# Performance work log

Hardware: AMD Instinct MI355X
Metric: run time of the kernel (lower is better)

The kernel has to match this reference:

```python
import jax, jax.numpy as jnp
import numpy as np

B, T, E, H, NH, L, R, K, N, P, HOR = 32, 16, 768, 1024, 16, 6, 8, 16, 100000, 9, 8
HD = H // NH


def _ln(x, g, b):
    m = jnp.mean(x, -1, keepdims=True)
    v = jnp.mean((x - m) ** 2, -1, keepdims=True)
    return (x - m) * jax.lax.rsqrt(v + 1e-5) * g + b


def _lora(x, W, A, Bm, b):
    # base linear + low-rank update: x W^T + (x A^T) B^T + b
    return x @ W.T + (x @ A.T) @ Bm.T + b


def setup_inputs() -> dict:
    key = jax.random.key(0)
    ks = iter(jax.random.split(key, 64))
    def rn(shape, s):
        return jax.random.normal(next(ks), shape, dtype=jnp.float32) * s
    d = {}
    d['history_img_emb'] = rn((B, T, E), 1.0)
    d['current_emb'] = rn((B, E), 1.0)
    d['goal_emb'] = rn((B, E), 1.0)
    d['subgoal_emb'] = rn((B, E), 1.0)
    d['beacon_emb'] = rn((B, E), 1.0)
    d['history_proprio'] = rn((B, T, P), 1.0)
    d['proprio'] = rn((B, P), 1.0)
    d['bank'] = rn((N, E), 1.0)
    d['hp_W'] = rn((H, E + P), 0.02); d['hp_b'] = jnp.zeros((H,), jnp.float32)
    d['ip_W'] = rn((H, E), 0.02); d['ip_b'] = jnp.zeros((H,), jnp.float32)
    d['pp_W'] = rn((H, P), 0.02); d['pp_b'] = jnp.zeros((H,), jnp.float32)
    d['plan_token'] = rn((1, 1, H), 0.02)
    d['ln1_g'] = jnp.ones((L, H), jnp.float32); d['ln1_b'] = jnp.zeros((L, H), jnp.float32)
    d['ln2_g'] = jnp.ones((L, H), jnp.float32); d['ln2_b'] = jnp.zeros((L, H), jnp.float32)
    for nm, o, i in (('q', H, H), ('k', H, H), ('v', H, H), ('o', H, H), ('f1', 4 * H, H), ('f2', H, 4 * H)):
        d[nm + 'W'] = rn((L, o, i), 0.02)
        d[nm + 'A'] = rn((L, R, i), 0.02)
        d[nm + 'B'] = rn((L, o, R), 0.02)
        d[nm + 'b'] = jnp.zeros((L, o), jnp.float32)
    d['fln_g'] = jnp.ones((H,), jnp.float32); d['fln_b'] = jnp.zeros((H,), jnp.float32)
    d['ah_W1'] = rn((H, H), 0.02); d['ah_b1'] = jnp.zeros((H,), jnp.float32)
    d['ah_W2'] = rn((3, H), 0.02); d['ah_b2'] = jnp.zeros((3,), jnp.float32)
    d['rh_W1'] = rn((H, H + 3), 0.02); d['rh_b1'] = jnp.zeros((H,), jnp.float32)
    d['rh_W2'] = rn((HOR * 3, H), 0.02); d['rh_b2'] = jnp.zeros((HOR * 3,), jnp.float32)
    d['sh_W'] = rn((1, H), 0.02); d['sh_b'] = jnp.zeros((1,), jnp.float32)
    return d


def reference(history_img_emb, current_emb, goal_emb, subgoal_emb, beacon_emb,
              history_proprio, proprio, bank,
              hp_W, hp_b, ip_W, ip_b, pp_W, pp_b, plan_token,
              ln1_g, ln1_b, ln2_g, ln2_b,
              qW, qA, qB, qb, kW, kA, kB, kb, vW, vA, vB, vb, oW, oA, oB, ob,
              f1W, f1A, f1B, f1b, f2W, f2A, f2B, f2b,
              fln_g, fln_b, ah_W1, ah_b1, ah_W2, ah_b2,
              rh_W1, rh_b1, rh_W2, rh_b2, sh_W, sh_b):
    # batched semantic-bank top-k retrieval (replaces the per-sample python loop)
    sims = current_emb @ bank.T                      # [B, N]
    scores, idx = jax.lax.top_k(sims, K)             # [B, K]
    sem = bank[idx] * scores[..., None]              # [B, K, E] gather + scale

    # multi-modal token fusion
    hist = jnp.concatenate([history_img_emb, history_proprio], -1) @ hp_W.T + hp_b  # [B, T, H]
    img = lambda e: e @ ip_W.T + ip_b
    goal_t = img(goal_emb)[:, None]
    sub_t = img(subgoal_emb)[:, None]
    bea_t = img(beacon_emb)[:, None]
    sem_t = img(sem)                                 # [B, K, H]
    prop_t = (proprio @ pp_W.T + pp_b)[:, None]
    plan_t = jnp.broadcast_to(plan_token, (B, 1, H))
    x = jnp.concatenate([plan_t, hist, goal_t, sub_t, bea_t, sem_t, prop_t], 1)  # [B, S=37, H]

    scale = 1.0 / np.sqrt(HD).astype(np.float32)
    for l in range(L):
        h = _ln(x, ln1_g[l], ln1_b[l])
        q = _lora(h, qW[l], qA[l], qB[l], qb[l]).reshape(B, -1, NH, HD)
        k = _lora(h, kW[l], kA[l], kB[l], kb[l]).reshape(B, -1, NH, HD)
        v = _lora(h, vW[l], vA[l], vB[l], vb[l]).reshape(B, -1, NH, HD)
        attn = jax.nn.softmax(jnp.einsum('bshd,bthd->bhst', q, k) * scale, axis=-1)
        out = jnp.einsum('bhst,bthd->bshd', attn, v).reshape(B, -1, H)
        x = x + _lora(out, oW[l], oA[l], oB[l], ob[l])
        h2 = _ln(x, ln2_g[l], ln2_b[l])
        x = x + _lora(jax.nn.gelu(_lora(h2, f1W[l], f1A[l], f1B[l], f1b[l]), approximate=False),
                      f2W[l], f2A[l], f2B[l], f2b[l])

    x = _ln(x, fln_g, fln_b)
    ps = x[:, 0]                                     # plan token state [B, H]
    anchor = jax.nn.gelu(ps @ ah_W1.T + ah_b1, approximate=False) @ ah_W2.T + ah_b2  # [B, 3]
    ref_in = jnp.concatenate([ps, anchor], -1)
    waypoints = (jax.nn.gelu(ref_in @ rh_W1.T + rh_b1, approximate=False) @ rh_W2.T + rh_b2).reshape(B, HOR, 3)
    stop_logit = (ps @ sh_W.T + sh_b)[:, 0]          # [B]
    return anchor, waypoints, stop_logit
```

## Files before the change

### kernel.cpp

```cpp
#include <hip/hip_runtime.h>
#include <float.h>
#include <math.h>

#define NB 100000
#define SEQ 37
#define NTOK 1184
#define TKCH 16

typedef __attribute__((ext_vector_type(8))) short short8;
typedef __attribute__((ext_vector_type(4))) float floatx4;

__device__ __forceinline__ short f2bf(float f) {
  union { float f; unsigned u; } x; x.f = f;
  unsigned r = x.u + 0x7fff + ((x.u >> 16) & 1);
  return (short)(r >> 16);
}

__device__ __forceinline__ float gelu_f(float v) {
  return 0.5f * v * (1.f + erff(v * 0.70710678118654752f));
}

__global__ __launch_bounds__(256) void wconv_all(const float* __restrict__ qW,
                                                 const float* __restrict__ kW,
                                                 const float* __restrict__ vW,
                                                 const float* __restrict__ oW,
                                                 const float* __restrict__ f1W,
                                                 const float* __restrict__ f2W,
                                                 short* __restrict__ wb) {
  const int l = blockIdx.x / 1536;
  const int t = blockIdx.x - l * 1536;
  const float* src; int Kd; size_t doff; int np, kc;
  if (t < 512) {
    const int w = t >> 7, ti = t & 127;
    const float* base = (w == 0) ? qW : (w == 1) ? kW : (w == 2) ? vW : oW;
    src = base + (size_t)l * 1024 * 1024;
    Kd = 1024; np = ti >> 4; kc = ti & 15;
    doff = (size_t)w * 1048576 + ((size_t)np * 16 + kc) * 8192;
  } else if (t < 1024) {
    const int ti = t - 512;
    src = f1W + (size_t)l * 4096 * 1024;
    Kd = 1024; np = ti >> 4; kc = ti & 15;
    doff = (size_t)4 * 1048576 + ((size_t)np * 16 + kc) * 8192;
  } else {
    const int ti = t - 1024;
    src = f2W + (size_t)l * 1024 * 4096;
    Kd = 4096; np = ti >> 6; kc = ti & 63;
    doff = (size_t)8 * 1048576 + ((size_t)np * 64 + kc) * 8192;
  }
  short* dst = wb + (size_t)l * 12 * 1048576 + doff;
  const float* sp = src + (size_t)(np * 128) * Kd + kc * 64;
  const int tid = threadIdx.x;
#pragma unroll
  for (int q = 0; q < 4; ++q) {
    const int d = q * 256 + tid;
    const int row = d >> 3, slot = d & 7;
    const int ss = slot ^ (row & 7);
    const float* s = sp + (size_t)row * Kd + ss * 8;
    const float4 u0 = *(const float4*)s;
    const float4 u1 = *(const float4*)(s + 4);
    short8 v;
    v[0] = f2bf(u0.x); v[1] = f2bf(u0.y); v[2] = f2bf(u0.z); v[3] = f2bf(u0.w);
    v[4] = f2bf(u1.x); v[5] = f2bf(u1.y); v[6] = f2bf(u1.z); v[7] = f2bf(u1.w);
    *(short8*)(dst + (size_t)d * 8) = v;
  }
}

__global__ __launch_bounds__(256) void wconv_embed(const float* __restrict__ hpW,
                                                   const float* __restrict__ ipW,
                                                   short* __restrict__ wbe) {
  const int t = blockIdx.x;
  const float* src; int Kd, np, kc; size_t doff;
  if (t < 104) { src = hpW; Kd = 777; np = t / 13; kc = t - np * 13; doff = (size_t)t * 8192; }
  else { const int ti = t - 104; src = ipW; Kd = 768; np = ti / 12; kc = ti - np * 12;
         doff = (size_t)t * 8192; }
  short* dst = wbe + doff;
  const int tid = threadIdx.x;
#pragma unroll
  for (int q = 0; q < 4; ++q) {
    const int d = q * 256 + tid;
    const int row = d >> 3, slot = d & 7;
    const int ss = slot ^ (row & 7);
    const int gk0 = kc * 64 + ss * 8;
    const float* s = src + (size_t)(np * 128 + row) * Kd;
    short8 v;
#pragma unroll
    for (int e = 0; e < 8; ++e) v[e] = (gk0 + e < Kd) ? f2bf(s[gk0 + e]) : (short)0;
    *(short8*)(dst + (size_t)d * 8) = v;
  }
}

__global__ __launch_bounds__(256) void gemm_bt(const float* __restrict__ A, int lda,
                                               const short* __restrict__ WT, size_t wzstride,
                                               const float* __restrict__ b0,
                                               const float* __restrict__ b1,
                                               const float* __restrict__ b2,
                                               const float* __restrict__ LT,
                                               const float* __restrict__ B0,
                                               const float* __restrict__ B1,
                                               const float* __restrict__ B2,
                                               float* __restrict__ C, size_t czstride,
                                               int ldc, int M, int K,
                                               int acc_flag, int gelu_flag,
                                               int ksn, float* __restrict__ part) {
  __shared__ short Al[2][64 * 64];
  __shared__ short Wl[2][128 * 64];
  const int z = blockIdx.z;
  const int kidx = (ksn > 1) ? z : 0;
  const float* bias = (ksn > 1 || z == 0) ? b0 : (z == 1) ? b1 : b2;
  const float* Bz = (ksn > 1 || z == 0) ? B0 : (z == 1) ? B1 : B2;
  if (ksn == 1) C += (size_t)z * czstride;
  const int nkc_tot = K >> 6;
  const int nkc = nkc_tot / ksn;
  const short* wt = WT + (size_t)((ksn > 1) ? 0 : z) * wzstride +
                    ((size_t)blockIdx.y * nkc_tot + (size_t)kidx * nkc) * 8192;
  const int tid = threadIdx.x;
  const int wid = tid >> 6, lane = tid & 63;
  const int wr = wid >> 1, wc = wid & 1;
  const int bm = blockIdx.x * 64, bn = blockIdx.y * 128;
  const int arow = tid >> 2;
  const int s0 = (tid & 3) * 2;

  floatx4 acc[2][4];
#pragma unroll
  for (int i = 0; i < 2; ++i)
#pragma unroll
    for (int j = 0; j < 4; ++j)
#pragma unroll
      for (int r = 0; r < 4; ++r) acc[i][j][r] = 0.f;

  const int ga = bm + arow;
  const bool aok = ga < M;
  const float* ap = A + (size_t)ga * lda + (size_t)kidx * nkc * 64;
  const int aswz = arow & 7;

  float4 ar[4];
  short8 wreg[4];

#define LOAD_A(kc_)                                                        \
  {                                                                        \
    _Pragma("unroll") for (int j = 0; j < 2; ++j) {                        \
      const int slot = s0 + j;                                             \
      if (aok) {                                                           \
        ar[j * 2] = *(const float4*)(ap + (kc_)*64 + slot * 8);            \
        ar[j * 2 + 1] = *(const float4*)(ap + (kc_)*64 + slot * 8 + 4);    \
      } else {                                                             \
        ar[j * 2] = make_float4(0.f, 0.f, 0.f, 0.f);                      \
        ar[j * 2 + 1] = make_float4(0.f, 0.f, 0.f, 0.f);                  \
      }                                                                    \
    }                                                                      \
  }
#define LOAD_W(kc_)                                                        \
  {                                                                        \
    _Pragma("unroll") for (int it = 0; it < 4; ++it)                       \
        wreg[it] = *(const short8*)(wt + (size_t)(kc_)*8192 + (it * 256 + tid) * 8); \
  }
#define WRITE_A(buf_)                                                      \
  {                                                                        \
    _Pragma("unroll") for (int j = 0; j < 2; ++j) {                        \
      const int slot = s0 + j;                                             \
      short8 s;                                                            \
      s[0] = f2bf(ar[j * 2].x); s[1] = f2bf(ar[j * 2].y);                  \
      s[2] = f2bf(ar[j * 2].z); s[3] = f2bf(ar[j * 2].w);                  \
      s[4] = f2bf(ar[j * 2 + 1].x); s[5] = f2bf(ar[j * 2 + 1].y);          \
      s[6] = f2bf(ar[j * 2 + 1].z); s[7] = f2bf(ar[j * 2 + 1].w);          \
      *(short8*)&Al[buf_][arow * 64 + ((slot ^ aswz) << 3)] = s;           \
    }                                                                      \
  }
#define WRITE_W(buf_)                                                      \
  {                                                                        \
    _Pragma("unroll") for (int it = 0; it < 4; ++it)                       \
        *(short8*)&Wl[buf_][(it * 256 + tid) * 8] = wreg[it];              \
  }

  LOAD_W(0) LOAD_A(0)
  WRITE_A(0) WRITE_W(0)
  __syncthreads();

  for (int t = 0; t < nkc; ++t) {
    const int cur = t & 1, nxt = cur ^ 1;
    const bool more = (t + 1 < nkc);
    if (more) { LOAD_W(t + 1) LOAD_A(t + 1) }
#pragma unroll
    for (int ks = 0; ks < 2; ++ks) {
      short8 af[2], wf[4];
#pragma unroll
      for (int i = 0; i < 2; ++i) {
        const int row = wr * 32 + i * 16 + (lane & 15);
        const int sa = (ks * 4 + (lane >> 4)) ^ (row & 7);
        af[i] = *(const short8*)&Al[cur][row * 64 + sa * 8];
      }
#pragma unroll
      for (int j = 0; j < 4; ++j) {
        const int col = wc * 64 + j * 16 + (lane & 15);
        const int sw2 = (ks * 4 + (lane >> 4)) ^ (col & 7);
        wf[j] = *(const short8*)&Wl[cur][col * 64 + sw2 * 8];
      }
#pragma unroll
      for (int i = 0; i < 2; ++i)
#pragma unroll
        for (int j = 0; j < 4; ++j)
          acc[i][j] = __builtin_amdgcn_mfma_f32_16x16x32_bf16(af[i], wf[j], acc[i][j], 0, 0, 0);
    }
    if (more) { WRITE_A(nxt) WRITE_W(nxt) }
    __syncthreads();
  }
#undef LOAD_A
#undef LOAD_W
#undef WRITE_A
#undef WRITE_W

  if (ksn > 1) {
#pragma unroll
    for (int i = 0; i < 2; ++i) {
      const int gm0 = bm + wr * 32 + i * 16 + (lane >> 4) * 4;
#pragma unroll
      for (int r = 0; r < 4; ++r) {
        const int gm = gm0 + r;
        if (gm >= M) continue;
#pragma unroll
        for (int j = 0; j < 4; ++j) {
          const int gn = bn + wc * 64 + j * 16 + (lane & 15);
          part[((size_t)kidx * M + gm) * ldc + gn] = acc[i][j][r];
        }
      }
    }
    return;
  }

  float br[4][8];
  if (LT) {
#pragma unroll
    for (int j = 0; j < 4; ++j) {
      const int gn = bn + wc * 64 + j * 16 + (lane & 15);
      const float4 u0 = *(const float4*)(Bz + (size_t)gn * 8);
      const float4 u1 = *(const float4*)(Bz + (size_t)gn * 8 + 4);
      br[j][0] = u0.x; br[j][1] = u0.y; br[j][2] = u0.z; br[j][3] = u0.w;
      br[j][4] = u1.x; br[j][5] = u1.y; br[j][6] = u1.z; br[j][7] = u1.w;
    }
  }
#pragma unroll
  for (int i = 0; i < 2; ++i) {
    const int gm0 = bm + wr * 32 + i * 16 + (lane >> 4) * 4;
#pragma unroll
    for (int r = 0; r < 4; ++r) {
      const int gm = gm0 + r;
      if (gm >= M) continue;
      float lt[8];
      if (LT) {
        const float4 t0 = *(const float4*)(LT + ((size_t)z * NTOK + gm) * 8);
        const float4 t1 = *(const float4*)(LT + ((size_t)z * NTOK + gm) * 8 + 4);
        lt[0] = t0.x; lt[1] = t0.y; lt[2] = t0.z; lt[3] = t0.w;
        lt[4] = t1.x; lt[5] = t1.y; lt[6] = t1.z; lt[7] = t1.w;
      }
#pragma unroll
      for (int j = 0; j < 4; ++j) {
        const int gn = bn + wc * 64 + j * 16 + (lane & 15);
        float o = acc[i][j][r] + bias[gn];
        if (LT)
          o += lt[0] * br[j][0] + lt[1] * br[j][1] + lt[2] * br[j][2] + lt[3] * br[j][3] +
               lt[4] * br[j][4] + lt[5] * br[j][5] + lt[6] * br[j][6] + lt[7] * br[j][7];
        const size_t off = (size_t)gm * ldc + gn;
        if (acc_flag) o += C[off];
        if (gelu_flag) o = gelu_f(o);
        C[off] = o;
      }
    }
  }
}

__global__ __launch_bounds__(256) void reduce_ks(const float* __restrict__ part,
                                                 const float* __restrict__ bias,
                                                 const float* __restrict__ LT,
                                                 const float* __restrict__ Bm,
                                                 float* __restrict__ X, int KS) {
  const int idx = blockIdx.x * 256 + threadIdx.x;
  if (idx >= NTOK * 1024) return;
  const int gm = idx >> 10, gn = idx & 1023;
  float s = 0.f;
  for (int h = 0; h < KS; ++h) s += part[(size_t)h * NTOK * 1024 + idx];
  const float* t = LT + (size_t)gm * 8;
  const float* bp = Bm + (size_t)gn * 8;
  s += t[0] * bp[0] + t[1] * bp[1] + t[2] * bp[2] + t[3] * bp[3] +
       t[4] * bp[4] + t[5] * bp[5] + t[6] * bp[6] + t[7] * bp[7];
  X[idx] += s + bias[gn];
}

__global__ __launch_bounds__(256) void redln(const float* __restrict__ part, int KS,
                                             const float* __restrict__ bias,
                                             const float* __restrict__ Bm,
                                             float* __restrict__ X,
                                             float* __restrict__ out,
                                             const float* __restrict__ g,
                                             const float* __restrict__ bt,
                                             const float* __restrict__ A0,
                                             const float* __restrict__ A1,
                                             const float* __restrict__ A2,
                                             int nz, float* __restrict__ lt) {
  __shared__ float red[4];
  __shared__ float red2[4][8];
  const int row = blockIdx.x, tid = threadIdx.x;
  const int wave = tid >> 6, lane = tid & 63;
  float ltv[8];
  {
    const float4 t0 = *(const float4*)(lt + (size_t)row * 8);
    const float4 t1 = *(const float4*)(lt + (size_t)row * 8 + 4);
    ltv[0] = t0.x; ltv[1] = t0.y; ltv[2] = t0.z; ltv[3] = t0.w;
    ltv[4] = t1.x; ltv[5] = t1.y; ltv[6] = t1.z; ltv[7] = t1.w;
  }
  float v[4];
#pragma unroll
  for (int i = 0; i < 4; ++i) {
    const int c = tid + 256 * i;
    float s = 0.f;
    for (int h = 0; h < KS; ++h)
      s += part[((size_t)h * NTOK + row) * 1024 + c];
    const float* bp = Bm + (size_t)c * 8;
    s += ltv[0] * bp[0] + ltv[1] * bp[1] + ltv[2] * bp[2] + ltv[3] * bp[3] +
         ltv[4] * bp[4] + ltv[5] * bp[5] + ltv[6] * bp[6] + ltv[7] * bp[7];
    float xnew = X[(size_t)row * 1024 + c] + s + bias[c];
    X[(size_t)row * 1024 + c] = xnew;
    v[i] = xnew;
  }
  float sum = v[0] + v[1] + v[2] + v[3];
#pragma unroll
  for (int s = 32; s; s >>= 1) sum += __shfl_down(sum, s);
  if ((tid & 63) == 0) red[tid >> 6] = sum;
  __syncthreads();
  float mean = (red[0] + red[1] + red[2] + red[3]) * (1.f / 1024.f);
  __syncthreads();
  float sq = 0.f;
#pragma unroll
  for (int i = 0; i < 4; ++i) { float d = v[i] - mean; sq += d * d; }
#pragma unroll
  for (int s = 32; s; s >>= 1) sq += __shfl_down(sq, s);
  if ((tid & 63) == 0) red[tid >> 6] = sq;
  __syncthreads();
  float var = (red[0] + red[1] + red[2] + red[3]) * (1.f / 1024.f);
  float inv = rsqrtf(var + 1e-5f);
  float* orow = out + (size_t)row * 1024;
  float nv[4];
#pragma unroll
  for (int i = 0; i < 4; ++i) {
    const int c = tid + 256 * i;
    nv[i] = (v[i] - mean) * inv * g[c] + bt[c];
    orow[c] = nv[i];
  }
  __syncthreads();
  for (int z = 0; z < nz; ++z) {
    const float* Am = (z == 0) ? A0 : (z == 1) ? A1 : A2;
    float p[8];
#pragma unroll
    for (int r = 0; r < 8; ++r) {
      float s = 0.f;
#pragma unroll
      for (int i = 0; i < 4; ++i) s += nv[i] * Am[r * 1024 + tid + 256 * i];
      p[r] = s;
    }
#pragma unroll
    for (int sh = 1; sh < 64; sh <<= 1) {
#pragma unroll
      for (int r = 0; r < 8; ++r) p[r] += __shfl_xor(p[r], sh);
    }
    if (lane == 0) {
#pragma unroll
      for (int r = 0; r < 8; ++r) red2[wave][r] = p[r];
    }
    __syncthreads();
    if (tid < 8)
      lt[((size_t)z * NTOK + row) * 8 + tid] =
          red2[0][tid] + red2[1][tid] + red2[2][tid] + red2[3][tid];
    __syncthreads();
  }
}

__global__ __launch_bounds__(256) void gemm_sm2(const float* __restrict__ A, int lda,
                                                const float* __restrict__ W, int ldw,
                                                const float* __restrict__ bias,
                                                float* __restrict__ C, int ldc,
                                                float* __restrict__ part,
                                                int N, int K, int gelu_flag) {
  __shared__ float buf[8192];
  const int tid = threadIdx.x;
  const int col = tid >> 3, ksub = tid & 7;
  const int gcol = blockIdx.x * 32 + col;
  const int KS = gridDim.y, ky = blockIdx.y;
  const int kchunk = (((K + KS - 1) / KS) + 127) & ~127;
  const int kstart = ky * kchunk;
  const int kend = (kstart + kchunk < K) ? (kstart + kchunk) : K;
  const float* wp = W + (size_t)(gcol < N ? gcol : 0) * ldw;

  float acc[32];
#pragma unroll
  for (int m = 0; m < 32; ++m) acc[m] = 0.f;

  for (int kc = kstart; kc < kend; kc += 128) {
    __syncthreads();
#pragma unroll
    for (int q = 0; q < 4; ++q) {
      const int idx4 = q * 256 + tid;
      const int m = idx4 >> 5, j = (idx4 & 31) * 4;
      const int gk = kc + j;
      float4 v;
      if (gk + 3 < K) {
        v = *(const float4*)(A + (size_t)m * lda + gk);
      } else {
        v.x = (gk < K) ? A[(size_t)m * lda + gk] : 0.f;
        v.y = (gk + 1 < K) ? A[(size_t)m * lda + gk + 1] : 0.f;
        v.z = (gk + 2 < K) ? A[(size_t)m * lda + gk + 2] : 0.f;
        v.w = (gk + 3 < K) ? A[(size_t)m * lda + gk + 3] : 0.f;
      }
      *(float4*)&buf[m * 128 + j] = v;
    }
    __syncthreads();
#pragma unroll
    for (int kk = 0; kk < 4; ++kk) {
      const int j = kk * 32 + ksub * 4;
      const int gk = kc + j;
      float4 w4 = make_float4(0.f, 0.f, 0.f, 0.f);
      if (gcol < N && gk < K) {
        if (gk + 3 < K) {
          w4 = *(const float4*)(wp + gk);
        } else {
          w4.x = wp[gk];
          if (gk + 1 < K) w4.y = wp[gk + 1];
          if (gk + 2 < K) w4.z = wp[gk + 2];
        }
      }
#pragma unroll
      for (int m = 0; m < 32; ++m) {
        const float4 a4 = *(const float4*)&buf[m * 128 + j];
        acc[m] += a4.x * w4.x + a4.y * w4.y + a4.z * w4.z + a4.w * w4.w;
      }
    }
  }
  __syncthreads();
#pragma unroll
  for (int m = 0; m < 32; ++m) buf[m * 256 + ksub * 32 + col] = acc[m];
  __syncthreads();
#pragma unroll
  for (int g = 0; g < 4; ++g) {
    const int idx = g * 256 + tid;
    const int m = idx >> 5, c = idx & 31;
    float s = 0.f;
#pragma unroll
    for (int h = 0; h < 8; ++h) s += buf[m * 256 + h * 32 + c];
    const int gc = blockIdx.x * 32 + c;
    if (gc < N) {
      if (KS == 1) {
        float o = s + bias[gc];
        if (gelu_flag) o = gelu_f(o);
        C[(size_t)m * ldc + gc] = o;
      } else {
        part[((size_t)ky * 32 + m) * N + gc] = s;
      }
    }
  }
}

__global__ __launch_bounds__(256) void reduce_sm(const float* __restrict__ part,
                                                 const float* __restrict__ bias,
                                                 float* __restrict__ C, int ldc,
                                                 int N, int KS, int gelu_flag) {
  const int idx = blockIdx.x * 256 + threadIdx.x;
  if (idx >= 32 * N) return;
  const int m = idx / N, c = idx - m * N;
  float s = 0.f;
  for (int h = 0; h < KS; ++h) s += part[((size_t)h * 32 + m) * N + c];
  float o = s + bias[c];
  if (gelu_flag) o = gelu_f(o);
  C[(size_t)m * ldc + c] = o;
}

__global__ __launch_bounds__(256) void sims_kernel(const float* __restrict__ cur,
                                                   const float* __restrict__ bank,
                                                   float* __restrict__ sims) {
  __shared__ float Bs[32][132];
  __shared__ float Cs[32][36];
  const int tid = threadIdx.x;
  const int tx = tid & 7;
  const int ty = tid >> 3;
  const int n0 = blockIdx.x * 128;
  const int srow = tid >> 1;
  const int spart = tid & 1;
  const int cb = tid >> 3;
  const int ck = (tid & 7) * 4;

  float acc[4][4] = {{0.f,0.f,0.f,0.f},{0.f,0.f,0.f,0.f},
                     {0.f,0.f,0.f,0.f},{0.f,0.f,0.f,0.f}};

  const bool rok = (n0 + srow) < NB;
  const float* bp = bank + (size_t)(n0 + srow) * 768 + spart * 16;
  const float* cp = cur + (size_t)cb * 768 + ck;

  for (int kc = 0; kc < 768; kc += 32) {
    __syncthreads();
#pragma unroll
    for (int jj = 0; jj < 4; ++jj) {
      float4 v = rok ? *(const float4*)(bp + kc + jj * 4)
                     : make_float4(0.f, 0.f, 0.f, 0.f);
      const int kk = spart * 16 + jj * 4;
      Bs[kk + 0][srow] = v.x; Bs[kk + 1][srow] = v.y;
      Bs[kk + 2][srow] = v.z; Bs[kk + 3][srow] = v.w;
    }
    {
      float4 v = *(const float4*)(cp + kc);
      Cs[ck + 0][cb] = v.x; Cs[ck + 1][cb] = v.y;
      Cs[ck + 2][cb] = v.z; Cs[ck + 3][cb] = v.w;
    }
    __syncthreads();
#pragma unroll
    for (int kk = 0; kk < 32; ++kk) {
      float4 av = *(const float4*)&Bs[kk][ty * 4];
      float4 bv = *(const float4*)&Cs[kk][tx * 4];
      float a4[4] = {av.x, av.y, av.z, av.w};
      float b4[4] = {bv.x, bv.y, bv.z, bv.w};
#pragma unroll
      for (int i = 0; i < 4; ++i)
#pragma unroll
        for (int j = 0; j < 4; ++j) acc[i][j] += a4[i] * b4[j];
    }
  }
  const int n = n0 + ty * 4;
#pragma unroll
  for (int j = 0; j < 4; ++j) {
    const int b = tx * 4 + j;
    float4 o = make_float4(acc[0][j], acc[1][j], acc[2][j], acc[3][j]);
    if (n + 3 < NB) {
      *(float4*)(sims + (size_t)b * NB + n) = o;
    } else {
      float oo[4] = {o.x, o.y, o.z, o.w};
      for (int i = 0; i < 4; ++i)
        if (n + i < NB) sims[(size_t)b * NB + n + i] = oo[i];
    }
  }
}

__global__ __launch_bounds__(256) void topk_stage1(const float* __restrict__ sims,
                                                   float* __restrict__ cv,
                                                   int* __restrict__ ci) {
  __shared__ float ss[4096];
  __shared__ int si[4096];
  __shared__ float wv[4];
  __shared__ int wi[4];
  const int chunk = blockIdx.x, b = blockIdx.y, tid = threadIdx.x;
  const int start = chunk * (NB / TKCH), end = start + (NB / TKCH);
  float ls[16]; int li[16];
#pragma unroll
  for (int i = 0; i < 16; ++i) { ls[i] = -FLT_MAX; li[i] = 0x7fffffff; }
  const float* row = sims + (size_t)b * NB;
  float lmin = -FLT_MAX;
  for (int n = start + tid; n < end; n += 256) {
    float v = row[n];
    if (v > lmin) {
      int p = 15;
      while (p > 0 && ls[p - 1] < v) { ls[p] = ls[p - 1]; li[p] = li[p - 1]; --p; }
      ls[p] = v; li[p] = n;
      lmin = ls[15];
    }
  }
#pragma unroll
  for (int i = 0; i < 16; ++i) { ss[i * 256 + tid] = ls[i]; si[i * 256 + tid] = li[i]; }
  __syncthreads();
  for (int round = 0; round < 16; ++round) {
    float bv = -FLT_MAX; int bi = 0x7fffffff;
#pragma unroll
    for (int i = 0; i < 16; ++i) {
      float v = ss[i * 256 + tid]; int ix = si[i * 256 + tid];
      if (v > bv || (v == bv && ix < bi)) { bv = v; bi = ix; }
    }
#pragma unroll
    for (int s = 32; s; s >>= 1) {
      float ov = __shfl_down(bv, s); int oi = __shfl_down(bi, s);
      if (ov > bv || (ov == bv && oi < bi)) { bv = ov; bi = oi; }
    }
    if ((tid & 63) == 0) { wv[tid >> 6] = bv; wi[tid >> 6] = bi; }
    __syncthreads();
    if (tid == 0) {
      bv = wv[0]; bi = wi[0];
      for (int w = 1; w < 4; ++w)
        if (wv[w] > bv || (wv[w] == bv && wi[w] < bi)) { bv = wv[w]; bi = wi[w]; }
      cv[(b * TKCH + chunk) * 16 + round] = bv;
      ci[(b * TKCH + chunk) * 16 + round] = bi;
      wi[0] = bi;
    }
    __syncthreads();
    bi = wi[0];
#pragma unroll
    for (int i = 0; i < 16; ++i)
      if (si[i * 256 + tid] == bi) ss[i * 256 + tid] = -FLT_MAX;
    __syncthreads();
  }
}

__global__ __launch_bounds__(256) void topk_stage2(const float* __restrict__ cv,
                                                   const int* __restrict__ ci,
                                                   float* __restrict__ tks,
                                                   int* __restrict__ tki) {
  __shared__ float wv[4];
  __shared__ int wi[4];
  __shared__ int bw;
  const int b = blockIdx.x, tid = threadIdx.x;
  float val = cv[b * 256 + tid];
  int idx = ci[b * 256 + tid];
  for (int round = 0; round < 16; ++round) {
    float bv = val; int bi = idx;
#pragma unroll
    for (int s = 1; s < 64; s <<= 1) {
      float ov = __shfl_xor(bv, s); int oi = __shfl_xor(bi, s);
      if (ov > bv || (ov == bv && oi < bi)) { bv = ov; bi = oi; }
    }
    if ((tid & 63) == 0) { wv[tid >> 6] = bv; wi[tid >> 6] = bi; }
    __syncthreads();
    if (tid == 0) {
      bv = wv[0]; bi = wi[0];
      for (int w = 1; w < 4; ++w)
        if (wv[w] > bv || (wv[w] == bv && wi[w] < bi)) { bv = wv[w]; bi = wi[w]; }
      tks[b * 16 + round] = bv; tki[b * 16 + round] = bi;
      bw = bi;
    }
    __syncthreads();
    if (idx == bw) val = -FLT_MAX;
  }
}

__global__ void sem_kernel(const float* __restrict__ bank, const float* __restrict__ tks,
                           const int* __restrict__ tki, float* __restrict__ sem) {
  int slot = blockIdx.x;
  float s = tks[slot]; int idx = tki[slot];
  for (int i = threadIdx.x; i < 768; i += 256)
    sem[(size_t)slot * 768 + i] = bank[(size_t)idx * 768 + i] * s;
}

__global__ void build_hist_in(const float* __restrict__ img, const float* __restrict__ pr,
                              float* __restrict__ out) {
  int r = blockIdx.x;
  for (int i = threadIdx.x; i < 832; i += 256)
    out[(size_t)r * 832 + i] = (i < 768) ? img[(size_t)r * 768 + i]
                             : (i < 777) ? pr[r * 9 + (i - 768)] : 0.f;
}

__global__ void build_img_in(const float* __restrict__ goal, const float* __restrict__ sub,
                             const float* __restrict__ bea, float* __restrict__ out) {
  int r = blockIdx.x;
  const float* src = (r < 32) ? goal + (size_t)r * 768
                   : (r < 64) ? sub + (size_t)(r - 32) * 768
                              : bea + (size_t)(r - 64) * 768;
  for (int i = threadIdx.x; i < 768; i += 256) out[(size_t)r * 768 + i] = src[i];
}

__global__ void assemble_x(const float* __restrict__ th, const float* __restrict__ ti,
                           const float* __restrict__ tp, const float* __restrict__ plan,
                           float* __restrict__ x) {
  int r = blockIdx.x;
  int b = r / SEQ, tok = r - b * SEQ;
  const float* src;
  if (tok == 0) src = plan;
  else if (tok <= 16) src = th + (size_t)(b * 16 + tok - 1) * 1024;
  else if (tok <= 19) src = ti + (size_t)((tok - 17) * 32 + b) * 1024;
  else if (tok <= 35) src = ti + (size_t)(96 + b * 16 + (tok - 20)) * 1024;
  else src = tp + (size_t)b * 1024;
  for (int i = threadIdx.x; i < 1024; i += 256) x[(size_t)r * 1024 + i] = src[i];
}

__global__ void build_ref(const float* __restrict__ ps, const float* __restrict__ anc,
                          float* __restrict__ ref) {
  int b = blockIdx.x;
  for (int i = threadIdx.x; i < 1027; i += 256)
    ref[(size_t)b * 1027 + i] = (i < 1024) ? ps[(size_t)b * 1024 + i] : anc[b * 3 + (i - 1024)];
}

__device__ __forceinline__ float block_sum256(float v, float* red) {
#pragma unroll
  for (int s = 32; s; s >>= 1) v += __shfl_down(v, s);
  if ((threadIdx.x & 63) == 0) red[threadIdx.x >> 6] = v;
  __syncthreads();
  float tot = red[0] + red[1] + red[2] + red[3];
  __syncthreads();
  return tot;
}

__global__ __launch_bounds__(256) void ln_kernel(const float* __restrict__ in, int in_stride,
                                                 float* __restrict__ out,
                                                 const float* __restrict__ g,
                                                 const float* __restrict__ bt,
                                                 const float* __restrict__ A0,
                                                 const float* __restrict__ A1,
                                                 const float* __restrict__ A2,
                                                 int nz, float* __restrict__ lt) {
  __shared__ float red[4];
  __shared__ float red2[4][8];
  const float* xr = in + (size_t)blockIdx.x * in_stride;
  const int tid = threadIdx.x;
  const int wave = tid >> 6, lane = tid & 63;
  float v[4];
#pragma unroll
  for (int i = 0; i < 4; ++i) v[i] = xr[tid + 256 * i];
  float mean = block_sum256(v[0] + v[1] + v[2] + v[3], red) * (1.f / 1024.f);
  float sq = 0.f;
#pragma unroll
  for (int i = 0; i < 4; ++i) { float d = v[i] - mean; sq += d * d; }
  float var = block_sum256(sq, red) * (1.f / 1024.f);
  float inv = rsqrtf(var + 1e-5f);
  float* orow = out + (size_t)blockIdx.x * 1024;
  float nv[4];
#pragma unroll
  for (int i = 0; i < 4; ++i) {
    int c = tid + 256 * i;
    nv[i] = (v[i] - mean) * inv * g[c] + bt[c];
    orow[c] = nv[i];
  }
  for (int z = 0; z < nz; ++z) {
    const float* Am = (z == 0) ? A0 : (z == 1) ? A1 : A2;
    float p[8];
#pragma unroll
    for (int r = 0; r < 8; ++r) {
      float s = 0.f;
#pragma unroll
      for (int i = 0; i < 4; ++i) s += nv[i] * Am[r * 1024 + tid + 256 * i];
      p[r] = s;
    }
#pragma unroll
    for (int sh = 1; sh < 64; sh <<= 1) {
#pragma unroll
      for (int r = 0; r < 8; ++r) p[r] += __shfl_xor(p[r], sh);
    }
    if (lane == 0) {
#pragma unroll
      for (int r = 0; r < 8; ++r) red2[wave][r] = p[r];
    }
    __syncthreads();
    if (tid < 8)
      lt[((size_t)z * NTOK + blockIdx.x) * 8 + tid] =
          red2[0][tid] + red2[1][tid] + red2[2][tid] + red2[3][tid];
    __syncthreads();
  }
}

__global__ __launch_bounds__(256) void lora_down(const float* __restrict__ h,
                                                 const float* __restrict__ A0,
                                                 const float* __restrict__ A1,
                                                 const float* __restrict__ A2,
                                                 float* __restrict__ lt, int K) {
  __shared__ float red[4][8];
  const int m = blockIdx.x, z = blockIdx.y;
  const int tid = threadIdx.x, wave = tid >> 6, lane = tid & 63;
  const float* A = (z == 0) ? A0 : (z == 1) ? A1 : A2;
  float p[8] = {0.f, 0.f, 0.f, 0.f, 0.f, 0.f, 0.f, 0.f};
  for (int kk = tid; kk < K; kk += 256) {
    float hv = h[(size_t)m * K + kk];
#pragma unroll
    for (int r = 0; r < 8; ++r) p[r] += hv * A[r * K + kk];
  }
#pragma unroll
  for (int s = 1; s < 64; s <<= 1) {
#pragma unroll
    for (int r = 0; r < 8; ++r) p[r] += __shfl_xor(p[r], s);
  }
  if (lane == 0) {
#pragma unroll
    for (int r = 0; r < 8; ++r) red[wave][r] = p[r];
  }
  __syncthreads();
  if (tid < 8)
    lt[((size_t)z * NTOK + m) * 8 + tid] =
        red[0][tid] + red[1][tid] + red[2][tid] + red[3][tid];
}

__global__ __launch_bounds__(256) void attn_kernel(const float* __restrict__ q,
                                                   const float* __restrict__ k,
                                                   const float* __restrict__ v,
                                                   float* __restrict__ ao) {
  __shared__ float qs[SEQ * 64], ks[SEQ * 64], vs[SEQ * 64], sc[SEQ * 40];
  const int head = blockIdx.x, b = blockIdx.y, tid = threadIdx.x;
  const size_t base = ((size_t)b * SEQ) * 1024 + head * 64;
  for (int i = tid; i < SEQ * 64; i += 256) {
    int s = i >> 6, d = i & 63;
    size_t off = base + (size_t)s * 1024 + d;
    qs[i] = q[off]; ks[i] = k[off]; vs[i] = v[off];
  }
  __syncthreads();
  for (int p = tid; p < SEQ * SEQ; p += 256) {
    int s = p / SEQ, t = p - s * SEQ;
    float acc = 0.f;
#pragma unroll 16
    for (int d = 0; d < 64; ++d) acc += qs[s * 64 + d] * ks[t * 64 + d];
    sc[s * 40 + t] = acc * 0.125f;
  }
  __syncthreads();
  if (tid < SEQ) {
    float m = -FLT_MAX;
    for (int t = 0; t < SEQ; ++t) m = fmaxf(m, sc[tid * 40 + t]);
    float sum = 0.f;
    for (int t = 0; t < SEQ; ++t) { float e = expf(sc[tid * 40 + t] - m); sc[tid * 40 + t] = e; sum += e; }
    float inv = 1.f / sum;
    for (int t = 0; t < SEQ; ++t) sc[tid * 40 + t] *= inv;
  }
  __syncthreads();
  for (int i = tid; i < SEQ * 64; i += 256) {
    int s = i >> 6, d = i & 63;
    float acc = 0.f;
    for (int t = 0; t < SEQ; ++t) acc += sc[s * 40 + t] * vs[t * 64 + d];
    ao[base + (size_t)s * 1024 + d] = acc;
  }
}

extern "C" void kernel_launch(void* const* d_in, const int* in_sizes, int n_in,
                              void* d_out, int out_size, void* d_ws, size_t ws_size,
                              hipStream_t stream) {
  const float* hist_img = (const float*)d_in[0];
  const float* cur      = (const float*)d_in[1];
  const float* goal     = (const float*)d_in[2];
  const float* sub      = (const float*)d_in[3];
  const float* bea      = (const float*)d_in[4];
  const float* hist_pr  = (const float*)d_in[5];
  const float* prop     = (const float*)d_in[6];
  const float* bank     = (const float*)d_in[7];
  const float* hpW = (const float*)d_in[8];  const float* hpb = (const float*)d_in[9];
  const float* ipW = (const float*)d_in[10]; const float* ipb = (const float*)d_in[11];
  const float* ppW = (const float*)d_in[12]; const float* ppb = (const float*)d_in[13];
  const float* plan = (const float*)d_in[14];
  const float* ln1g = (const float*)d_in[15]; const float* ln1b = (const float*)d_in[16];
  const float* ln2g = (const float*)d_in[17]; const float* ln2b = (const float*)d_in[18];
  const float* qW = (const float*)d_in[19]; const float* qA = (const float*)d_in[20];
  const float* qB = (const float*)d_in[21]; const float* qb = (const float*)d_in[22];
  const float* kW = (const float*)d_in[23]; const float* kA = (const float*)d_in[24];
  const float* kB = (const float*)d_in[25]; const float* kb = (const float*)d_in[26];
  const float* vW = (const float*)d_in[27]; const float* vA = (const float*)d_in[28];
  const float* vB = (const float*)d_in[29]; const float* vb = (const float*)d_in[30];
  const float* oW = (const float*)d_in[31]; const float* oA = (const float*)d_in[32];
  const float* oB = (const float*)d_in[33]; const float* ob = (const float*)d_in[34];
  const float* f1W = (const float*)d_in[35]; const float* f1A = (const float*)d_in[36];
  const float* f1B = (const float*)d_in[37]; const float* f1b = (const float*)d_in[38];
  const float* f2W = (const float*)d_in[39]; const float* f2A = (const float*)d_in[40];
  const float* f2B = (const float*)d_in[41]; const float* f2b = (const float*)d_in[42];
  const float* flng = (const float*)d_in[43]; const float* flnb = (const float*)d_in[44];
  const float* ahW1 = (const float*)d_in[45]; const float* ahb1 = (const float*)d_in[46];
  const float* ahW2 = (const float*)d_in[47]; const float* ahb2 = (const float*)d_in[48];
  const float* rhW1 = (const float*)d_in[49]; const float* rhb1 = (const float*)d_in[50];
  const float* rhW2 = (const float*)d_in[51]; const float* rhb2 = (const float*)d_in[52];
  const float* shW = (const float*)d_in[53]; const float* shb = (const float*)d_in[54];
  float* out = (float*)d_out;

  float* ws  = (float*)d_ws;
  float* F1O = ws;
  float* SIMS = ws;
  float* X   = F1O + (size_t)NTOK * 4096;
  float* Hb  = X  + (size_t)NTOK * 1024;
  float* Qb  = Hb + (size_t)NTOK * 1024;
  float* Kb  = Qb + (size_t)NTOK * 1024;
  float* Vb  = Kb + (size_t)NTOK * 1024;
  float* AOb = Vb + (size_t)NTOK * 1024;
  float* LT  = AOb + (size_t)NTOK * 1024;
  float* SEM = LT + (size_t)3 * NTOK * 8;
  float* HIN = SEM + (size_t)512 * 768;
  float* TKS = HIN + (size_t)512 * 832;
  int*   TKI = (int*)(TKS + 512);
  float* PS  = TKS + 1024;
  float* HH  = PS + 32 * 1024;
  float* REF = HH + 32 * 1024;
  float* CV  = REF + 32 * 1027;
  int*   CI  = (int*)(CV + 32 * 256);
  float* PART = (float*)(CI + 32 * 256);
  float* PF2 = PART + 8 * 32 * 1024;
  short* WB  = (short*)(PF2 + (size_t)4 * NTOK * 1024);
  short* WBE = WB + (size_t)6 * 12 * 1048576;

  const size_t czs = (size_t)NTOK * 1024;
  const size_t WM = 1048576;
  const size_t WL = 12 * WM;

  auto gemms = [&](const float* A, int lda, const float* W, int ldw, const float* bias,
                   float* C, int ldc, int N, int K, int geluf, int KS) {
    gemm_sm2<<<dim3((N + 31) / 32, KS), 256, 0, stream>>>(A, lda, W, ldw, bias,
                                                          C, ldc, PART, N, K, geluf);
    if (KS > 1)
      reduce_sm<<<(32 * N + 255) / 256, 256, 0, stream>>>(PART, bias, C, ldc, N, KS, geluf);
  };

  wconv_all<<<6 * 1536, 256, 0, stream>>>(qW, kW, vW, oW, f1W, f2W, WB);
  wconv_embed<<<200, 256, 0, stream>>>(hpW, ipW, WBE);

  sims_kernel<<<(NB + 127) / 128, 256, 0, stream>>>(cur, bank, SIMS);
  topk_stage1<<<dim3(TKCH, 32), 256, 0, stream>>>(SIMS, CV, CI);
  topk_stage2<<<32, 256, 0, stream>>>(CV, CI, TKS, TKI);
  sem_kernel<<<512, 256, 0, stream>>>(bank, TKS, TKI, AOb + (size_t)96 * 768);

  build_hist_in<<<512, 256, 0, stream>>>(hist_img, hist_pr, HIN);
  build_img_in<<<96, 256, 0, stream>>>(goal, sub, bea, AOb);
  gemm_bt<<<dim3(8, 8, 1), 256, 0, stream>>>(
      HIN, 832, WBE, 0, hpb, hpb, hpb,
      nullptr, nullptr, nullptr, nullptr, Qb, 0, 1024, 512, 832, 0, 0, 1, nullptr);
  gemm_bt<<<dim3(10, 8, 1), 256, 0, stream>>>(
      AOb, 768, WBE + (size_t)104 * 8192, 0, ipb, ipb, ipb,
      nullptr, nullptr, nullptr, nullptr, Kb, 0, 1024, 608, 768, 0, 0, 1, nullptr);
  gemms(prop, 9, ppW, 9, ppb, Vb, 1024, 1024, 9, 0, 1);
  assemble_x<<<NTOK, 256, 0, stream>>>(Qb, Kb, Vb, plan, X);

  const int mblk = (NTOK + 63) / 64;
  ln_kernel<<<NTOK, 256, 0, stream>>>(X, 1024, Hb, ln1g, ln1b, qA, kA, vA, 3, LT);
  for (int l = 0; l < 6; ++l) {
    const size_t aO = (size_t)l * 8 * 1024, bO = (size_t)l * 1024 * 8,
                 biO = (size_t)l * 1024;
    const size_t a4O = (size_t)l * 8 * 4096, b4O = (size_t)l * 4096 * 8,
                 bi4O = (size_t)l * 4096;
    const short* WBl = WB + (size_t)l * WL;
    gemm_bt<<<dim3(mblk, 8, 3), 256, 0, stream>>>(
        Hb, 1024, WBl, WM, qb + biO, kb + biO, vb + biO,
        LT, qB + bO, kB + bO, vB + bO, Qb, czs, 1024, NTOK, 1024, 0, 0, 1, nullptr);
    attn_kernel<<<dim3(16, 32), 256, 0, stream>>>(Qb, Kb, Vb, AOb);
    lora_down<<<dim3(NTOK, 1), 256, 0, stream>>>(AOb, oA + aO, oA + aO, oA + aO, LT, 1024);
    gemm_bt<<<dim3(mblk, 8, 2), 256, 0, stream>>>(
        AOb, 1024, WBl + 3 * WM, 0, ob + biO, ob + biO, ob + biO,
        nullptr, nullptr, nullptr, nullptr, nullptr, 0, 1024, NTOK, 1024, 0, 0, 2, PF2);
    redln<<<NTOK, 256, 0, stream>>>(PF2, 2, ob + biO, oB + bO, X, Hb,
                                    ln2g + biO, ln2b + biO,
                                    f1A + aO, f1A + aO, f1A + aO, 1, LT);
    gemm_bt<<<dim3(mblk, 32, 1), 256, 0, stream>>>(
        Hb, 1024, WBl + 4 * WM, 0, f1b + bi4O, f1b + bi4O, f1b + bi4O,
        LT, f1B + b4O, f1B + b4O, f1B + b4O, F1O, 0, 4096, NTOK, 1024, 0, 1, 1, nullptr);
    lora_down<<<dim3(NTOK, 1), 256, 0, stream>>>(F1O, f2A + a4O, f2A + a4O, f2A + a4O, LT, 4096);
    gemm_bt<<<dim3(mblk, 8, 4), 256, 0, stream>>>(
        F1O, 4096, WBl + 8 * WM, 0, f2b + biO, f2b + biO, f2b + biO,
        nullptr, nullptr, nullptr, nullptr, nullptr, 0, 1024, NTOK, 4096, 0, 0, 4, PF2);
    if (l < 5) {
      redln<<<NTOK, 256, 0, stream>>>(PF2, 4, f2b + biO, f2B + bO, X, Hb,
                                      ln1g + biO + 1024, ln1b + biO + 1024,
                                      qA + aO + 8192, kA + aO + 8192, vA + aO + 8192,
                                      3, LT);
    } else {
      reduce_ks<<<(NTOK * 1024 + 255) / 256, 256, 0, stream>>>(PF2, f2b + biO, LT,
                                                               f2B + bO, X, 4);
    }
  }

  ln_kernel<<<32, 256, 0, stream>>>(X, SEQ * 1024, PS, flng, flnb,
                                    nullptr, nullptr, nullptr, 0, nullptr);
  gemms(PS, 1024, ahW1, 1024, ahb1, HH, 1024, 1024, 1024, 1, 8);
  gemms(HH, 1024, ahW2, 1024, ahb2, out, 3, 3, 1024, 0, 8);
  build_ref<<<32, 256, 0, stream>>>(PS, out, REF);
  gemms(REF, 1027, rhW1, 1027, rhb1, HH, 1024, 1024, 1027, 1, 8);
  gemms(HH, 1024, rhW2, 1024, rhb2, out + 96, 24, 24, 1024, 0, 8);
  gemms(PS, 1024, shW, 1024, shb, out + 864, 1, 1, 1024, 0, 8);
}
```

Before: 1.688 ms.

## Scatter embedding GEMM outputs directly into sequence layout; warp-parallel attention softmax

Result: no change. 1.694 ms (+0.4%).

```diff
diff --git a/kernel.cpp b/kernel.cpp
--- a/kernel.cpp
+++ b/kernel.cpp
@@ -101,7 +101,8 @@
                                                float* __restrict__ C, size_t czstride,
                                                int ldc, int M, int K,
                                                int acc_flag, int gelu_flag,
-                                               int ksn, float* __restrict__ part) {
+                                               int ksn, float* __restrict__ part,
+                                               int rowmap) {
   __shared__ short Al[2][64 * 64];
   __shared__ short Wl[2][128 * 64];
   const int z = blockIdx.z;
@@ -252,6 +253,13 @@
         lt[0] = t0.x; lt[1] = t0.y; lt[2] = t0.z; lt[3] = t0.w;
         lt[4] = t1.x; lt[5] = t1.y; lt[6] = t1.z; lt[7] = t1.w;
       }
+      int xr = gm;
+      if (rowmap == 1) {
+        xr = (gm >> 4) * SEQ + 1 + (gm & 15);
+      } else if (rowmap == 2) {
+        if (gm < 96) xr = (gm & 31) * SEQ + 17 + (gm >> 5);
+        else { const int jj = gm - 96; xr = (jj >> 4) * SEQ + 20 + (jj & 15); }
+      }
 #pragma unroll
       for (int j = 0; j < 4; ++j) {
         const int gn = bn + wc * 64 + j * 16 + (lane & 15);
@@ -259,7 +267,7 @@
         if (LT)
           o += lt[0] * br[j][0] + lt[1] * br[j][1] + lt[2] * br[j][2] + lt[3] * br[j][3] +
                lt[4] * br[j][4] + lt[5] * br[j][5] + lt[6] * br[j][6] + lt[7] * br[j][7];
-        const size_t off = (size_t)gm * ldc + gn;
+        const size_t off = (size_t)xr * ldc + gn;
         if (acc_flag) o += C[off];
         if (gelu_flag) o = gelu_f(o);
         C[off] = o;
@@ -648,18 +656,10 @@
   for (int i = threadIdx.x; i < 768; i += 256) out[(size_t)r * 768 + i] = src[i];
 }
 
-__global__ void assemble_x(const float* __restrict__ th, const float* __restrict__ ti,
-                           const float* __restrict__ tp, const float* __restrict__ plan,
-                           float* __restrict__ x) {
-  int r = blockIdx.x;
-  int b = r / SEQ, tok = r - b * SEQ;
-  const float* src;
-  if (tok == 0) src = plan;
-  else if (tok <= 16) src = th + (size_t)(b * 16 + tok - 1) * 1024;
-  else if (tok <= 19) src = ti + (size_t)((tok - 17) * 32 + b) * 1024;
-  else if (tok <= 35) src = ti + (size_t)(96 + b * 16 + (tok - 20)) * 1024;
-  else src = tp + (size_t)b * 1024;
-  for (int i = threadIdx.x; i < 1024; i += 256) x[(size_t)r * 1024 + i] = src[i];
+__global__ void plan_fill(const float* __restrict__ plan, float* __restrict__ x) {
+  int b = blockIdx.x;
+  for (int i = threadIdx.x; i < 1024; i += 256)
+    x[((size_t)b * SEQ) * 1024 + i] = plan[i];
 }
 
 __global__ void build_ref(const float* __restrict__ ps, const float* __restrict__ anc,
@@ -772,6 +772,7 @@
                                                    float* __restrict__ ao) {
   __shared__ float qs[SEQ * 64], ks[SEQ * 64], vs[SEQ * 64], sc[SEQ * 40];
   const int head = blockIdx.x, b = blockIdx.y, tid = threadIdx.x;
+  const int wave = tid >> 6, lane = tid & 63;
   const size_t base = ((size_t)b * SEQ) * 1024 + head * 64;
   for (int i = tid; i < SEQ * 64; i += 256) {
     int s = i >> 6, d = i & 63;
@@ -787,13 +788,16 @@
     sc[s * 40 + t] = acc * 0.125f;
   }
   __syncthreads();
-  if (tid < SEQ) {
-    float m = -FLT_MAX;
-    for (int t = 0; t < SEQ; ++t) m = fmaxf(m, sc[tid * 40 + t]);
-    float sum = 0.f;
-    for (int t = 0; t < SEQ; ++t) { float e = expf(sc[tid * 40 + t] - m); sc[tid * 40 + t] = e; sum += e; }
-    float inv = 1.f / sum;
-    for (int t = 0; t < SEQ; ++t) sc[tid * 40 + t] *= inv;
+  for (int r = wave; r < SEQ; r += 4) {
+    float val = (lane < SEQ) ? sc[r * 40 + lane] : -FLT_MAX;
+    float m = val;
+#pragma unroll
+    for (int s = 32; s; s >>= 1) m = fmaxf(m, __shfl_xor(m, s));
+    float e = (lane < SEQ) ? expf(val - m) : 0.f;
+    float sum = e;
+#pragma unroll
+    for (int s = 32; s; s >>= 1) sum += __shfl_xor(sum, s);
+    if (lane < SEQ) sc[r * 40 + lane] = e / sum;
   }
   __syncthreads();
   for (int i = tid; i < SEQ * 64; i += 256) {
@@ -864,6 +868,7 @@
   float* PF2 = PART + 8 * 32 * 1024;
   short* WB  = (short*)(PF2 + (size_t)4 * NTOK * 1024);
   short* WBE = WB + (size_t)6 * 12 * 1048576;
+  float* IMGIN = AOb;
 
   const size_t czs = (size_t)NTOK * 1024;
   const size_t WM = 1048576;
@@ -883,18 +888,18 @@
   sims_kernel<<<(NB + 127) / 128, 256, 0, stream>>>(cur, bank, SIMS);
   topk_stage1<<<dim3(TKCH, 32), 256, 0, stream>>>(SIMS, CV, CI);
   topk_stage2<<<32, 256, 0, stream>>>(CV, CI, TKS, TKI);
-  sem_kernel<<<512, 256, 0, stream>>>(bank, TKS, TKI, AOb + (size_t)96 * 768);
+  sem_kernel<<<512, 256, 0, stream>>>(bank, TKS, TKI, IMGIN + (size_t)96 * 768);
 
   build_hist_in<<<512, 256, 0, stream>>>(hist_img, hist_pr, HIN);
-  build_img_in<<<96, 256, 0, stream>>>(goal, sub, bea, AOb);
+  build_img_in<<<96, 256, 0, stream>>>(goal, sub, bea, IMGIN);
+  plan_fill<<<32, 256, 0, stream>>>(plan, X);
   gemm_bt<<<dim3(8, 8, 1), 256, 0, stream>>>(
       HIN, 832, WBE, 0, hpb, hpb, hpb,
-      nullptr, nullptr, nullptr, nullptr, Qb, 0, 1024, 512, 832, 0, 0, 1, nullptr);
+      nullptr, nullptr, nullptr, nullptr, X, 0, 1024, 512, 832, 0, 0, 1, nullptr, 1);
   gemm_bt<<<dim3(10, 8, 1), 256, 0, stream>>>(
-      AOb, 768, WBE + (size_t)104 * 8192, 0, ipb, ipb, ipb,
-      nullptr, nullptr, nullptr, nullptr, Kb, 0, 1024, 608, 768, 0, 0, 1, nullptr);
-  gemms(prop, 9, ppW, 9, ppb, Vb, 1024, 1024, 9, 0, 1);
-  assemble_x<<<NTOK, 256, 0, stream>>>(Qb, Kb, Vb, plan, X);
+      IMGIN, 768, WBE + (size_t)104 * 8192, 0, ipb, ipb, ipb,
+      nullptr, nullptr, nullptr, nullptr, X, 0, 1024, 608, 768, 0, 0, 1, nullptr, 2);
+  gemms(prop, 9, ppW, 9, ppb, X + (size_t)36 * 1024, SEQ * 1024, 1024, 9, 0, 1);
 
   const int mblk = (NTOK + 63) / 64;
   ln_kernel<<<NTOK, 256, 0, stream>>>(X, 1024, Hb, ln1g, ln1b, qA, kA, vA, 3, LT);
@@ -906,22 +911,22 @@
     const short* WBl = WB + (size_t)l * WL;
     gemm_bt<<<dim3(mblk, 8, 3), 256, 0, stream>>>(
         Hb, 1024, WBl, WM, qb + biO, kb + biO, vb + biO,
-        LT, qB + bO, kB + bO, vB + bO, Qb, czs, 1024, NTOK, 1024, 0, 0, 1, nullptr);
+        LT, qB + bO, kB + bO, vB + bO, Qb, czs, 1024, NTOK, 1024, 0, 0, 1, nullptr, 0);
     attn_kernel<<<dim3(16, 32), 256, 0, stream>>>(Qb, Kb, Vb, AOb);
     lora_down<<<dim3(NTOK, 1), 256, 0, stream>>>(AOb, oA + aO, oA + aO, oA + aO, LT, 1024);
     gemm_bt<<<dim3(mblk, 8, 2), 256, 0, stream>>>(
         AOb, 1024, WBl + 3 * WM, 0, ob + biO, ob + biO, ob + biO,
-        nullptr, nullptr, nullptr, nullptr, nullptr, 0, 1024, NTOK, 1024, 0, 0, 2, PF2);
+        nullptr, nullptr, nullptr, nullptr, nullptr, 0, 1024, NTOK, 1024, 0, 0, 2, PF2, 0);
     redln<<<NTOK, 256, 0, stream>>>(PF2, 2, ob + biO, oB + bO, X, Hb,
                                     ln2g + biO, ln2b + biO,
                                     f1A + aO, f1A + aO, f1A + aO, 1, LT);
     gemm_bt<<<dim3(mblk, 32, 1), 256, 0, stream>>>(
         Hb, 1024, WBl + 4 * WM, 0, f1b + bi4O, f1b + bi4O, f1b + bi4O,
-        LT, f1B + b4O, f1B + b4O, f1B + b4O, F1O, 0, 4096, NTOK, 1024, 0, 1, 1, nullptr);
+        LT, f1B + b4O, f1B + b4O, f1B + b4O, F1O, 0, 4096, NTOK, 1024, 0, 1, 1, nullptr, 0);
     lora_down<<<dim3(NTOK, 1), 256, 0, stream>>>(F1O, f2A + a4O, f2A + a4O, f2A + a4O, LT, 4096);
     gemm_bt<<<dim3(mblk, 8, 4), 256, 0, stream>>>(
         F1O, 4096, WBl + 8 * WM, 0, f2b + biO, f2b + biO, f2b + biO,
-        nullptr, nullptr, nullptr, nullptr, nullptr, 0, 1024, NTOK, 4096, 0, 0, 4, PF2);
+        nullptr, nullptr, nullptr, nullptr, nullptr, 0, 1024, NTOK, 4096, 0, 0, 4, PF2, 0);
     if (l < 5) {
       redln<<<NTOK, 256, 0, stream>>>(PF2, 4, f2b + biO, f2B + bO, X, Hb,
                                       ln1g + biO + 1024, ln1b + biO + 1024,
```
